# Performance work log

Measured on AMD Instinct MI355X. Metric: run time of the kernel, lower is better.

Reference implementation:

```python
import jax, jax.numpy as jnp
import numpy as np

B, T, D, H = 8, 2048, 512, 2048
EPS = 1e-5


def setup_inputs() -> dict:
    key = jax.random.key(0)
    ks = jax.random.split(key, 12)
    s_d = 1.0 / np.sqrt(D)
    s_h = 1.0 / np.sqrt(H)
    s_w = np.sqrt(6.0 / (T + T))  # xavier_uniform scale for w [T,T]
    return {
        "x": jax.random.normal(ks[0], (B, T, D), jnp.float32),
        "ln1_g": jnp.ones((D,), jnp.float32),
        "ln1_b": jnp.zeros((D,), jnp.float32),
        "Wk": jax.random.normal(ks[1], (D, D), jnp.float32) * s_d,
        "bk": jnp.zeros((D,), jnp.float32),
        "Wv": jax.random.normal(ks[2], (D, D), jnp.float32) * s_d,
        "bv": jnp.zeros((D,), jnp.float32),
        "Wq": jax.random.normal(ks[3], (D, D), jnp.float32) * s_d,
        "bq": jnp.zeros((D,), jnp.float32),
        "w": jax.random.uniform(ks[4], (T, T), jnp.float32, -s_w, s_w),
        "Wo": jax.random.normal(ks[5], (D, D), jnp.float32) * s_d,
        "bo": jnp.zeros((D,), jnp.float32),
        "ln2_g": jnp.ones((D,), jnp.float32),
        "ln2_b": jnp.zeros((D,), jnp.float32),
        "W1": jax.random.normal(ks[6], (D, H), jnp.float32) * s_d,
        "b1": jnp.zeros((H,), jnp.float32),
        "W2": jax.random.normal(ks[7], (H, D), jnp.float32) * s_h,
        "b2": jnp.zeros((D,), jnp.float32),
    }


def _ln(x, g, b):
    mu = jnp.mean(x, axis=-1, keepdims=True)
    var = jnp.mean(jnp.square(x - mu), axis=-1, keepdims=True)
    return (x - mu) * jax.lax.rsqrt(var + EPS) * g + b


def _aft_full(h, Wk, bk, Wv, bv, Wq, bq, w, Wo, bo):
    # h: [B,T,D]
    K = h @ Wk + bk
    V = h @ Wv + bv
    # row-max stabilized position bias [T,T]
    exp_w = jnp.exp(w - jnp.max(w, axis=-1, keepdims=True))
    # NOTE: original stabilizes K with max over dim=0 (the BATCH dim) -- faithful
    exp_K = jnp.exp(K - jnp.max(K, axis=0, keepdims=True))  # [B,T,D]
    num = jnp.einsum("ts,bsd->btd", exp_w, exp_K * V)
    den = jnp.einsum("ts,bsd->btd", exp_w, exp_K)
    Yt = num / den
    Q = h @ Wq + bq
    Yt = jax.nn.sigmoid(Q) * Yt
    return Yt @ Wo + bo


def reference(x, ln1_g, ln1_b, Wk, bk, Wv, bv, Wq, bq, w, Wo, bo,
              ln2_g, ln2_b, W1, b1, W2, b2):
    attn = _aft_full(_ln(x, ln1_g, ln1_b), Wk, bk, Wv, bv, Wq, bq, w, Wo, bo)
    out = attn + x
    h = _ln(out, ln2_g, ln2_b)
    h = jax.nn.gelu(h @ W1 + b1, approximate=False)
    h = jax.nn.gelu(h @ W2 + b2, approximate=False)  # GELU after 2nd linear too (faithful)
    return h + out
```

## Files before the change

### kernel.cpp

```cpp
#include <hip/hip_runtime.h>
#include <hip/hip_bf16.h>
#include <math.h>

typedef __hip_bfloat16 bf16;
typedef __bf16 bf16x8 __attribute__((ext_vector_type(8)));
typedef float f32x4 __attribute__((ext_vector_type(4)));

#define B_ 8
#define T_ 2048
#define D_ 512
#define H_ 2048

__device__ __forceinline__ float b2f(unsigned short u) {
    return __uint_as_float((unsigned)u << 16);
}
__device__ __forceinline__ float ldf(const float* p, long i) { return p[i]; }
__device__ __forceinline__ float ldf(const bf16* p, long i) {
    return b2f(((const unsigned short*)p)[i]);
}
__device__ __forceinline__ float gelu_f(float v) {
    float a = 1.5957691216057308f * (v + 0.044715f * v * v * v);
    return v / (1.0f + __expf(-a));
}

#define GLD16(g, l)                                                          \
    __builtin_amdgcn_global_load_lds(                                        \
        (const __attribute__((address_space(1))) void*)(g),                  \
        (__attribute__((address_space(3))) void*)(l), 16, 0, 0)

template <typename Tin>
__global__ __launch_bounds__(256) void ln_kernel(const Tin* __restrict__ x,
                                                 const float* __restrict__ g,
                                                 const float* __restrict__ bb,
                                                 bf16* __restrict__ y) {
    long base = (long)blockIdx.x * D_;
    int tid = threadIdx.x;
    float v0 = ldf(x, base + tid);
    float v1 = ldf(x, base + tid + 256);
    float s = v0 + v1;
#pragma unroll
    for (int off = 32; off > 0; off >>= 1) s += __shfl_down(s, off);
    __shared__ float red[4];
    int lane = tid & 63, wid = tid >> 6;
    if (lane == 0) red[wid] = s;
    __syncthreads();
    float mean = (red[0] + red[1] + red[2] + red[3]) * (1.0f / 512.0f);
    __syncthreads();
    float d0 = v0 - mean, d1 = v1 - mean;
    float vs = d0 * d0 + d1 * d1;
#pragma unroll
    for (int off = 32; off > 0; off >>= 1) vs += __shfl_down(vs, off);
    if (lane == 0) red[wid] = vs;
    __syncthreads();
    float var = (red[0] + red[1] + red[2] + red[3]) * (1.0f / 512.0f);
    float rstd = rsqrtf(var + 1e-5f);
    y[base + tid]       = __float2bfloat16(d0 * rstd * g[tid]       + bb[tid]);
    y[base + tid + 256] = __float2bfloat16(d1 * rstd * g[tid + 256] + bb[tid + 256]);
}

__global__ __launch_bounds__(256) void expw_kernel(const float* __restrict__ w,
                                                   bf16* __restrict__ ew) {
    long base = (long)blockIdx.x * T_;
    int tid = threadIdx.x;
    float v[8];
    float mx = -3.4e38f;
#pragma unroll
    for (int i = 0; i < 8; ++i) {
        v[i] = w[base + tid + i * 256];
        mx = fmaxf(mx, v[i]);
    }
#pragma unroll
    for (int off = 32; off > 0; off >>= 1) mx = fmaxf(mx, __shfl_down(mx, off));
    __shared__ float red[4];
    if ((tid & 63) == 0) red[tid >> 6] = mx;
    __syncthreads();
    float rmax = fmaxf(fmaxf(red[0], red[1]), fmaxf(red[2], red[3]));
#pragma unroll
    for (int i = 0; i < 8; ++i)
        ew[base + tid + i * 256] = __float2bfloat16(expf(v[i] - rmax));
}

__global__ __launch_bounds__(256) void maxk_kernel(const bf16* __restrict__ K,
                                                   float* __restrict__ mk) {
    long i = (long)blockIdx.x * 256 + threadIdx.x;
    float m = ldf(K, i);
#pragma unroll
    for (int b = 1; b < B_; ++b) m = fmaxf(m, ldf(K, (long)b * (T_ * D_) + i));
    mk[i] = m;
}

__global__ __launch_bounds__(256) void kv2t_kernel(const bf16* __restrict__ K_,
                                                   const bf16* __restrict__ V_,
                                                   const float* __restrict__ mk,
                                                   bf16* __restrict__ kv2t) {
    __shared__ float sev[64][65];
    __shared__ float se[64][65];
    int tx = threadIdx.x & 63, ty = threadIdx.x >> 6;
    int t0 = blockIdx.x * 64, d0 = blockIdx.y * 64, b = blockIdx.z;
    long ibase = (long)b << 20;
#pragma unroll
    for (int r = 0; r < 16; ++r) {
        int tl = r * 4 + ty;
        long mi = (long)(t0 + tl) * D_ + d0 + tx;
        float e = expf(ldf(K_, ibase + mi) - mk[mi]);
        sev[tl][tx] = e * ldf(V_, ibase + mi);
        se[tl][tx] = e;
    }
    __syncthreads();
    long obase = (long)b << 21;
#pragma unroll
    for (int r = 0; r < 16; ++r) {
        int dl = r * 4 + ty;
        kv2t[obase + (long)(d0 + dl) * T_ + t0 + tx]        = __float2bfloat16(sev[tx][dl]);
        kv2t[obase + (long)(512 + d0 + dl) * T_ + t0 + tx]  = __float2bfloat16(se[tx][dl]);
    }
}

__global__ __launch_bounds__(256) void yt_kernel(const bf16* __restrict__ nd,
                                                 bf16* __restrict__ q) {
    long i = (long)blockIdx.x * 256 + threadIdx.x;
    long td = i & (long)(T_ * D_ - 1);
    long b = i >> 20;
    long t = td >> 9;
    long d = td & (D_ - 1);
    long base = (b << 21) + (t << 10);
    float num = ldf(nd, base + d), den = ldf(nd, base + D_ + d);
    q[i] = __float2bfloat16(ldf(q, i) * num / den);
}

struct WT6 {
    const float* src[6];
    bf16* dst[6];
    int K[6], N[6];
};
__global__ __launch_bounds__(256) void wtrans6_kernel(WT6 p) {
    int z = blockIdx.z;
    int K = p.K[z], N = p.N[z];
    int n0 = blockIdx.x * 64, k0 = blockIdx.y * 64;
    if (n0 >= N || k0 >= K) return;
    const float* W = p.src[z];
    bf16* WT = p.dst[z];
    __shared__ float s[64][65];
    int tx = threadIdx.x & 63, ty = threadIdx.x >> 6;
#pragma unroll
    for (int r = 0; r < 16; ++r) {
        int kl = r * 4 + ty;
        s[kl][tx] = W[(long)(k0 + kl) * N + n0 + tx];
    }
    __syncthreads();
#pragma unroll
    for (int r = 0; r < 16; ++r) {
        int nl = r * 4 + ty;
        WT[(long)(n0 + nl) * K + k0 + tx] = __float2bfloat16(s[tx][nl]);
    }
}

template <int BM>
__global__ __launch_bounds__(256, 3) void mfma_gemm(
    const bf16* __restrict__ A, const bf16* __restrict__ Bt,
    const float* __restrict__ b0, const float* __restrict__ b1,
    const float* __restrict__ b2,
    bf16* __restrict__ Cb, float* __restrict__ Cf,
    const bf16* __restrict__ resb, const float* __restrict__ resf,
    int M, int N, int K, int modes, long bsB, long bsC, long planeStride) {
    constexpr int MI = BM / 32;
    constexpr int NA = BM / 64;
    constexpr int PL = (BM + 128) * 32;
    __shared__ short Sh[2 * PL];
    int tid = threadIdx.x;
    int lane = tid & 63, wave = tid >> 6;
    int wm = wave & 1, wn = wave >> 1;

    int gx = gridDim.x;
    int nwg = gx * gridDim.y;
    int o = blockIdx.x + gx * blockIdx.y;
    int wk = (o & 7) * (nwg >> 3) + (o >> 3);
    int bx = wk % gx, by = wk / gx;
    int m0 = by * BM, n0 = bx * 128;

    const short* Ag = (const short*)A;
    const short* Bg = (const short*)Bt + (long)blockIdx.z * bsB;

    int lr = lane >> 2;
    int le = (lane & 3) * 8;
    const short* ga[NA];
    short* la[NA];
#pragma unroll
    for (int i = 0; i < NA; ++i) {
        ga[i] = Ag + (long)(m0 + wave * (BM / 4) + i * 16 + lr) * K + le;
        la[i] = Sh + (wave * (BM / 4) + i * 16) * 32;
    }
    const short* gb0 = Bg + (long)(n0 + wave * 32 + lr) * K + le;
    const short* gb1 = gb0 + 16L * K;
    short* lb0 = Sh + BM * 32 + (wave * 32) * 32;
    short* lb1 = lb0 + 16 * 32;

    f32x4 acc[MI][4];
    f32x4 zz = {0.f, 0.f, 0.f, 0.f};
#pragma unroll
    for (int i = 0; i < MI; ++i)
#pragma unroll
        for (int j = 0; j < 4; ++j) acc[i][j] = zz;

    int fr = lane & 15;
    int fk = (lane >> 4) * 8;
    int rm = wm * (BM / 2);

    auto stage = [&](int kt, int ofs) {
        int ko = kt * 32;
#pragma unroll
        for (int i = 0; i < NA; ++i) GLD16(ga[i] + ko, la[i] + ofs);
        GLD16(gb0 + ko, lb0 + ofs);
        GLD16(gb1 + ko, lb1 + ofs);
    };
    auto compute = [&](int ofs) {
        const short* Asb = Sh + ofs;
        const short* Bsb = Sh + ofs + BM * 32;
        bf16x8 af[MI], bv[4];
#pragma unroll
        for (int mi = 0; mi < MI; ++mi)
            af[mi] = *(const bf16x8*)(Asb + (rm + mi * 16 + fr) * 32 + fk);
#pragma unroll
        for (int ni = 0; ni < 4; ++ni)
            bv[ni] = *(const bf16x8*)(Bsb + (wn * 64 + ni * 16 + fr) * 32 + fk);
#pragma unroll
        for (int mi = 0; mi < MI; ++mi)
#pragma unroll
            for (int ni = 0; ni < 4; ++ni)
                acc[mi][ni] = __builtin_amdgcn_mfma_f32_16x16x32_bf16(
                    af[mi], bv[ni], acc[mi][ni], 0, 0, 0);
    };

    int nk = K >> 5;
    stage(0, 0);
    __syncthreads();
    for (int kt = 0; kt < nk; kt += 2) {
        if (kt + 1 < nk) stage(kt + 1, PL);
        compute(0);
        __syncthreads();
        if (kt + 2 < nk) stage(kt + 2, 0);
        compute(PL);
        __syncthreads();
    }

    int cc = lane & 15, cr = (lane >> 4) * 4;
    long cbase = (long)blockIdx.z * bsC;
#pragma unroll
    for (int mi = 0; mi < MI; ++mi) {
#pragma unroll
        for (int ni = 0; ni < 4; ++ni) {
            int row0 = m0 + rm + mi * 16 + cr;
            int col = n0 + wn * 64 + ni * 16 + cc;
            float bvl;
            long colterm;
            int md, rowstride;
            if (planeStride) {
                int plane = col >> 9;
                int c2 = col & 511;
                const float* bp = (plane == 0) ? b0 : ((plane == 1) ? b1 : b2);
                bvl = bp[c2];
                md = (modes >> (2 * plane)) & 3;
                colterm = (long)plane * planeStride + c2;
                rowstride = 512;
            } else {
                bvl = b0 ? b0[col] : 0.0f;
                md = modes & 3;
                colterm = col;
                rowstride = N;
            }
#pragma unroll
            for (int r = 0; r < 4; ++r) {
                float v = acc[mi][ni][r] + bvl;
                if (md == 1) v = 1.0f / (1.0f + __expf(-v));
                else if (md == 2) v = gelu_f(v);
                long idx = cbase + (long)(row0 + r) * rowstride + colterm;
                if (resf) v += resf[idx];
                if (resb) v += ldf(resb, idx);
                if (Cf) Cf[idx] = v;
                else Cb[idx] = __float2bfloat16(v);
            }
        }
    }
}

extern "C" void kernel_launch(void* const* d_in, const int* in_sizes, int n_in,
                              void* d_out, int out_size, void* d_ws, size_t ws_size,
                              hipStream_t stream) {
    const float* x    = (const float*)d_in[0];
    const float* ln1g = (const float*)d_in[1];
    const float* ln1b = (const float*)d_in[2];
    const float* Wk   = (const float*)d_in[3];
    const float* bk   = (const float*)d_in[4];
    const float* Wv   = (const float*)d_in[5];
    const float* bv   = (const float*)d_in[6];
    const float* Wq   = (const float*)d_in[7];
    const float* bq   = (const float*)d_in[8];
    const float* w    = (const float*)d_in[9];
    const float* Wo   = (const float*)d_in[10];
    const float* bo   = (const float*)d_in[11];
    const float* ln2g = (const float*)d_in[12];
    const float* ln2b = (const float*)d_in[13];
    const float* W1   = (const float*)d_in[14];
    const float* b1   = (const float*)d_in[15];
    const float* W2   = (const float*)d_in[16];
    const float* b2   = (const float*)d_in[17];
    float* out = (float*)d_out;

    const long S_BTD = (long)B_ * T_ * D_;
    const long S_TD  = (long)T_ * D_;
    const long S_TT  = (long)T_ * T_;
    const long S_B2D = (long)B_ * T_ * 2 * D_;
    const long S_DD  = (long)D_ * D_;

    bf16* h1     = (bf16*)d_ws;
    bf16* outres = h1 + S_BTD;
    bf16* ew     = outres + S_BTD;
    bf16* KVQ    = ew + S_TT;
    bf16* kv2t   = KVQ + 3 * S_BTD;
    float* mk    = (float*)(kv2t + S_B2D);
    bf16* WkT    = (bf16*)(mk + S_TD);
    bf16* WvT    = WkT + S_DD;
    bf16* WqT    = WvT + S_DD;
    bf16* WoT    = WqT + S_DD;
    bf16* W1T    = WoT + S_DD;
    bf16* W2T    = W1T + (long)D_ * H_;
    bf16* Kb  = KVQ;
    bf16* Vb  = KVQ + S_BTD;
    bf16* Qb  = KVQ + 2 * S_BTD;
    bf16* nd  = KVQ;
    bf16* hH  = KVQ;
    bf16* h2  = h1;

    const int M = B_ * T_;

    WT6 p;
    p.src[0] = Wk; p.src[1] = Wv; p.src[2] = Wq; p.src[3] = Wo; p.src[4] = W1; p.src[5] = W2;
    p.dst[0] = WkT; p.dst[1] = WvT; p.dst[2] = WqT; p.dst[3] = WoT; p.dst[4] = W1T; p.dst[5] = W2T;
    p.K[0] = p.K[1] = p.K[2] = p.K[3] = 512; p.K[4] = 512; p.K[5] = 2048;
    p.N[0] = p.N[1] = p.N[2] = p.N[3] = 512; p.N[4] = 2048; p.N[5] = 512;
    wtrans6_kernel<<<dim3(32, 32, 6), 256, 0, stream>>>(p);
    ln_kernel<float><<<M, 256, 0, stream>>>(x, ln1g, ln1b, h1);
    mfma_gemm<128><<<dim3(1536 / 128, M / 128, 1), 256, 0, stream>>>(
        h1, WkT, bk, bv, bq, Kb, nullptr, nullptr, nullptr,
        M, 1536, D_, (1 << 4), 0, 0, S_BTD);
    maxk_kernel<<<S_TD / 256, 256, 0, stream>>>(Kb, mk);
    kv2t_kernel<<<dim3(T_ / 64, D_ / 64, B_), 256, 0, stream>>>(Kb, Vb, mk, kv2t);
    expw_kernel<<<T_, 256, 0, stream>>>(w, ew);
    mfma_gemm<128><<<dim3(1024 / 128, T_ / 128, B_), 256, 0, stream>>>(
        ew, kv2t, nullptr, nullptr, nullptr, nd, nullptr, nullptr, nullptr,
        T_, 1024, T_, 0, (long)1024 * T_, (long)T_ * 1024, 0);
    yt_kernel<<<S_BTD / 256, 256, 0, stream>>>(nd, Qb);
    mfma_gemm<128><<<dim3(D_ / 128, M / 128, 1), 256, 0, stream>>>(
        Qb, WoT, bo, nullptr, nullptr, outres, nullptr, nullptr, x,
        M, D_, D_, 0, 0, 0, 0);
    ln_kernel<bf16><<<M, 256, 0, stream>>>(outres, ln2g, ln2b, h2);
    mfma_gemm<128><<<dim3(H_ / 128, M / 128, 1), 256, 0, stream>>>(
        h2, W1T, b1, nullptr, nullptr, hH, nullptr, nullptr, nullptr,
        M, H_, D_, 2, 0, 0, 0);
    mfma_gemm<128><<<dim3(D_ / 128, M / 128, 1), 256, 0, stream>>>(
        hH, W2T, b2, nullptr, nullptr, nullptr, out, outres, nullptr,
        M, D_, H_, 2, 0, 0, 0);
}
```

Baseline: 504.9 us.

## Store GEMM operands in 16x32 packed tiles and remap grid swizzle over batch

Introduces a tiled packed layout (16 rows x 32 cols contiguous 1KB blocks) for GEMM operands written by layernorm, exp(w), kv transpose, weight transpose and the W1 GEMM epilogue. The GEMM loaders then read each 16x32 tile as one contiguous 1KB chunk per wave instead of 16 strided rows, which should improve DRAM/L2 access locality. The workgroup swizzle is also extended to include the batch dimension. In exchange, the producer kernels now do scattered stores, and every producer and consumer must agree on the layout.

```diff
diff --git a/kernel.cpp b/kernel.cpp
--- a/kernel.cpp
+++ b/kernel.cpp
@@ -23,17 +23,22 @@
     return v / (1.0f + __expf(-a));
 }
 
+__device__ __forceinline__ long poff(int row, int col, int K) {
+    return ((long)(row >> 4) * (K >> 5) + (col >> 5)) * 512 + (row & 15) * 32 + (col & 31);
+}
+
 #define GLD16(g, l)                                                          \
     __builtin_amdgcn_global_load_lds(                                        \
         (const __attribute__((address_space(1))) void*)(g),                  \
         (__attribute__((address_space(3))) void*)(l), 16, 0, 0)
 
-template <typename Tin>
+template <typename Tin, bool PACKO>
 __global__ __launch_bounds__(256) void ln_kernel(const Tin* __restrict__ x,
                                                  const float* __restrict__ g,
                                                  const float* __restrict__ bb,
                                                  bf16* __restrict__ y) {
-    long base = (long)blockIdx.x * D_;
+    int row = blockIdx.x;
+    long base = (long)row * D_;
     int tid = threadIdx.x;
     float v0 = ldf(x, base + tid);
     float v1 = ldf(x, base + tid + 256);
@@ -54,13 +59,21 @@
     __syncthreads();
     float var = (red[0] + red[1] + red[2] + red[3]) * (1.0f / 512.0f);
     float rstd = rsqrtf(var + 1e-5f);
-    y[base + tid]       = __float2bfloat16(d0 * rstd * g[tid]       + bb[tid]);
-    y[base + tid + 256] = __float2bfloat16(d1 * rstd * g[tid + 256] + bb[tid + 256]);
+    float o0 = d0 * rstd * g[tid] + bb[tid];
+    float o1 = d1 * rstd * g[tid + 256] + bb[tid + 256];
+    if (PACKO) {
+        y[poff(row, tid, D_)]       = __float2bfloat16(o0);
+        y[poff(row, tid + 256, D_)] = __float2bfloat16(o1);
+    } else {
+        y[base + tid]       = __float2bfloat16(o0);
+        y[base + tid + 256] = __float2bfloat16(o1);
+    }
 }
 
 __global__ __launch_bounds__(256) void expw_kernel(const float* __restrict__ w,
                                                    bf16* __restrict__ ew) {
-    long base = (long)blockIdx.x * T_;
+    int row = blockIdx.x;
+    long base = (long)row * T_;
     int tid = threadIdx.x;
     float v[8];
     float mx = -3.4e38f;
@@ -77,7 +90,7 @@
     float rmax = fmaxf(fmaxf(red[0], red[1]), fmaxf(red[2], red[3]));
 #pragma unroll
     for (int i = 0; i < 8; ++i)
-        ew[base + tid + i * 256] = __float2bfloat16(expf(v[i] - rmax));
+        ew[poff(row, tid + i * 256, T_)] = __float2bfloat16(expf(v[i] - rmax));
 }
 
 __global__ __launch_bounds__(256) void maxk_kernel(const bf16* __restrict__ K,
@@ -111,8 +124,8 @@
 #pragma unroll
     for (int r = 0; r < 16; ++r) {
         int dl = r * 4 + ty;
-        kv2t[obase + (long)(d0 + dl) * T_ + t0 + tx]        = __float2bfloat16(sev[tx][dl]);
-        kv2t[obase + (long)(512 + d0 + dl) * T_ + t0 + tx]  = __float2bfloat16(se[tx][dl]);
+        kv2t[obase + poff(d0 + dl, t0 + tx, T_)]       = __float2bfloat16(sev[tx][dl]);
+        kv2t[obase + poff(512 + d0 + dl, t0 + tx, T_)] = __float2bfloat16(se[tx][dl]);
     }
 }
 
@@ -151,7 +164,7 @@
 #pragma unroll
     for (int r = 0; r < 16; ++r) {
         int nl = r * 4 + ty;
-        WT[(long)(n0 + nl) * K + k0 + tx] = __float2bfloat16(s[tx][nl]);
+        WT[poff(n0 + nl, k0 + tx, K)] = __float2bfloat16(s[tx][nl]);
     }
 }
 
@@ -162,7 +175,7 @@
     const float* __restrict__ b2,
     bf16* __restrict__ Cb, float* __restrict__ Cf,
     const bf16* __restrict__ resb, const float* __restrict__ resf,
-    int M, int N, int K, int modes, long bsB, long bsC, long planeStride) {
+    int M, int N, int K, int modes, long bsB, long bsC, long planeStride, int pk) {
     constexpr int MI = BM / 32;
     constexpr int NA = BM / 64;
     constexpr int PL = (BM + 128) * 32;
@@ -171,15 +184,19 @@
     int lane = tid & 63, wave = tid >> 6;
     int wm = wave & 1, wn = wave >> 1;
 
-    int gx = gridDim.x;
-    int nwg = gx * gridDim.y;
-    int o = blockIdx.x + gx * blockIdx.y;
-    int wk = (o & 7) * (nwg >> 3) + (o >> 3);
-    int bx = wk % gx, by = wk / gx;
+    int gx = gridDim.x, gy = gridDim.y;
+    long nwg = (long)gx * gy * gridDim.z;
+    long o = blockIdx.x + (long)gx * (blockIdx.y + (long)gy * blockIdx.z);
+    long wk = (o & 7) * (nwg >> 3) + (o >> 3);
+    int bx = (int)(wk % gx);
+    long rq = wk / gx;
+    int by = (int)(rq % gy);
+    int bz = (int)(rq / gy);
     int m0 = by * BM, n0 = bx * 128;
 
+    const bool PA = pk & 1, PB = pk & 2, PCK = pk & 4;
     const short* Ag = (const short*)A;
-    const short* Bg = (const short*)Bt + (long)blockIdx.z * bsB;
+    const short* Bg = (const short*)Bt + (long)bz * bsB;
 
     int lr = lane >> 2;
     int le = (lane & 3) * 8;
@@ -187,13 +204,19 @@
     short* la[NA];
 #pragma unroll
     for (int i = 0; i < NA; ++i) {
-        ga[i] = Ag + (long)(m0 + wave * (BM / 4) + i * 16 + lr) * K + le;
+        int arow = m0 + wave * (BM / 4) + i * 16;
+        ga[i] = PA ? Ag + (long)(arow >> 4) * ((long)K << 4) + lane * 8
+                   : Ag + (long)(arow + lr) * K + le;
         la[i] = Sh + (wave * (BM / 4) + i * 16) * 32;
     }
-    const short* gb0 = Bg + (long)(n0 + wave * 32 + lr) * K + le;
-    const short* gb1 = gb0 + 16L * K;
+    int brow = n0 + wave * 32;
+    const short* gb0 = PB ? Bg + (long)(brow >> 4) * ((long)K << 4) + lane * 8
+                          : Bg + (long)(brow + lr) * K + le;
+    const short* gb1 = PB ? gb0 + ((long)K << 4) : gb0 + 16L * K;
     short* lb0 = Sh + BM * 32 + (wave * 32) * 32;
     short* lb1 = lb0 + 16 * 32;
+    const long astep = PA ? 512 : 32;
+    const long bstep = PB ? 512 : 32;
 
     f32x4 acc[MI][4];
     f32x4 zz = {0.f, 0.f, 0.f, 0.f};
@@ -207,11 +230,10 @@
     int rm = wm * (BM / 2);
 
     auto stage = [&](int kt, int ofs) {
-        int ko = kt * 32;
-#pragma unroll
-        for (int i = 0; i < NA; ++i) GLD16(ga[i] + ko, la[i] + ofs);
-        GLD16(gb0 + ko, lb0 + ofs);
-        GLD16(gb1 + ko, lb1 + ofs);
+#pragma unroll
+        for (int i = 0; i < NA; ++i) GLD16(ga[i] + kt * astep, la[i] + ofs);
+        GLD16(gb0 + kt * bstep, lb0 + ofs);
+        GLD16(gb1 + kt * bstep, lb1 + ofs);
     };
     auto compute = [&](int ofs) {
         const short* Asb = Sh + ofs;
@@ -244,7 +266,7 @@
     }
 
     int cc = lane & 15, cr = (lane >> 4) * 4;
-    long cbase = (long)blockIdx.z * bsC;
+    long cbase = (long)bz * bsC;
 #pragma unroll
     for (int mi = 0; mi < MI; ++mi) {
 #pragma unroll
@@ -273,7 +295,9 @@
                 float v = acc[mi][ni][r] + bvl;
                 if (md == 1) v = 1.0f / (1.0f + __expf(-v));
                 else if (md == 2) v = gelu_f(v);
-                long idx = cbase + (long)(row0 + r) * rowstride + colterm;
+                long idx;
+                if (PCK) idx = cbase + poff(row0 + r, col, N);
+                else     idx = cbase + (long)(row0 + r) * rowstride + colterm;
                 if (resf) v += resf[idx];
                 if (resb) v += ldf(resb, idx);
                 if (Cf) Cf[idx] = v;
@@ -339,25 +363,25 @@
     p.K[0] = p.K[1] = p.K[2] = p.K[3] = 512; p.K[4] = 512; p.K[5] = 2048;
     p.N[0] = p.N[1] = p.N[2] = p.N[3] = 512; p.N[4] = 2048; p.N[5] = 512;
     wtrans6_kernel<<<dim3(32, 32, 6), 256, 0, stream>>>(p);
-    ln_kernel<float><<<M, 256, 0, stream>>>(x, ln1g, ln1b, h1);
+    ln_kernel<float, true><<<M, 256, 0, stream>>>(x, ln1g, ln1b, h1);
     mfma_gemm<128><<<dim3(1536 / 128, M / 128, 1), 256, 0, stream>>>(
         h1, WkT, bk, bv, bq, Kb, nullptr, nullptr, nullptr,
-        M, 1536, D_, (1 << 4), 0, 0, S_BTD);
+        M, 1536, D_, (1 << 4), 0, 0, S_BTD, 3);
     maxk_kernel<<<S_TD / 256, 256, 0, stream>>>(Kb, mk);
     kv2t_kernel<<<dim3(T_ / 64, D_ / 64, B_), 256, 0, stream>>>(Kb, Vb, mk, kv2t);
     expw_kernel<<<T_, 256, 0, stream>>>(w, ew);
     mfma_gemm<128><<<dim3(1024 / 128, T_ / 128, B_), 256, 0, stream>>>(
         ew, kv2t, nullptr, nullptr, nullptr, nd, nullptr, nullptr, nullptr,
-        T_, 1024, T_, 0, (long)1024 * T_, (long)T_ * 1024, 0);
+        T_, 1024, T_, 0, (long)1024 * T_, (long)T_ * 1024, 0, 3);
     yt_kernel<<<S_BTD / 256, 256, 0, stream>>>(nd, Qb);
     mfma_gemm<128><<<dim3(D_ / 128, M / 128, 1), 256, 0, stream>>>(
         Qb, WoT, bo, nullptr, nullptr, outres, nullptr, nullptr, x,
-        M, D_, D_, 0, 0, 0, 0);
-    ln_kernel<bf16><<<M, 256, 0, stream>>>(outres, ln2g, ln2b, h2);
+        M, D_, D_, 0, 0, 0, 0, 2);
+    ln_kernel<bf16, true><<<M, 256, 0, stream>>>(outres, ln2g, ln2b, h2);
     mfma_gemm<128><<<dim3(H_ / 128, M / 128, 1), 256, 0, stream>>>(
         h2, W1T, b1, nullptr, nullptr, hH, nullptr, nullptr, nullptr,
-        M, H_, D_, 2, 0, 0, 0);
+        M, H_, D_, 2, 0, 0, 0, 7);
     mfma_gemm<128><<<dim3(D_ / 128, M / 128, 1), 256, 0, stream>>>(
         hH, W2T, b2, nullptr, nullptr, nullptr, out, outres, nullptr,
-        M, D_, H_, 2, 0, 0, 0);
-}
+        M, D_, H_, 2, 0, 0, 0, 3);
+}
```

After: 490.1 us. 2.9% less time.
